# Kernel optimization log

Measured on AMD Instinct MI355X. Metric: run time of the kernel, lower is better.

## Reference

```python
import jax, jax.numpy as jnp
import numpy as np

B, S, D, H = 2, 2048, 1024, 16
DK = D // H


def setup_inputs() -> dict:
    key = jax.random.key(0)
    ks = jax.random.split(key, 12)
    scale = 1.0 / np.sqrt(D)
    inp = {
        "query": jax.random.normal(ks[0], (B, S, D), jnp.float32),
        "key": jax.random.normal(ks[1], (B, S, D), jnp.float32),
        "value": jax.random.normal(ks[2], (B, S, D), jnp.float32),
        "mask": jax.random.randint(ks[3], (B, 1, S, S), 0, 2, jnp.int32),
        "Wq": jax.random.normal(ks[4], (D, D), jnp.float32) * scale,
        "bq": jnp.zeros((D,), jnp.float32),
        "Wk": jax.random.normal(ks[5], (D, D), jnp.float32) * scale,
        "bk": jnp.zeros((D,), jnp.float32),
        "Wv": jax.random.normal(ks[6], (D, D), jnp.float32) * scale,
        "bv": jnp.zeros((D,), jnp.float32),
        "Wo": jax.random.normal(ks[7], (D, D), jnp.float32) * scale,
        "bo": jnp.zeros((D,), jnp.float32),
    }
    return inp


def reference(query, key, value, mask, Wq, bq, Wk, bk, Wv, bv, Wo, bo):
    # Linear projections (dropout is identity in eval mode)
    q = query @ Wq + bq          # (B,S,D)
    k = key @ Wk + bk
    v = value @ Wv + bv

    # split heads: (B,S,D) -> (B,H,S,DK)
    def split(x):
        return x.reshape(B, S, H, DK).transpose(0, 2, 1, 3)

    q, k, v = split(q), split(k), split(v)

    scores = jnp.einsum("bhqd,bhkd->bhqk", q, k) / jnp.sqrt(jnp.float32(DK))
    scores = jnp.where(mask == 0, jnp.float32(-1e9), scores)
    p_attn = jax.nn.softmax(scores, axis=-1)   # (B,H,S,S)

    att = jnp.einsum("bhqk,bhkd->bhqd", p_attn, v)  # (B,H,S,DK)
    merged = att.transpose(0, 2, 1, 3).reshape(B, S, D)
    return merged @ Wo + bo
```

## Files before the change

kernel.cpp:

```cpp
#include <hip/hip_runtime.h>
#include <hip/hip_bf16.h>
#include <cstdint>
#include <cstddef>


#define B_ 2
#define S_ 2048
#define D_ 1024
#define H_ 16
#define M_ 4096

typedef unsigned short u16;
typedef __attribute__((ext_vector_type(8))) short bf16x8;
typedef __attribute__((ext_vector_type(8))) unsigned short u16x8;
typedef __attribute__((ext_vector_type(4))) unsigned short u16x4;
typedef __attribute__((ext_vector_type(4))) unsigned int u32x4;
typedef __attribute__((ext_vector_type(4))) float f32x4;
typedef __attribute__((ext_vector_type(4))) int i32x4;

#define QSCALE 0.18033688011112042f

__device__ __forceinline__ u16 f2bf(float f) {
  __hip_bfloat16 h = __float2bfloat16(f);
  return *reinterpret_cast<u16*>(&h);
}

__device__ __forceinline__ unsigned cvtpk(float lo, float hi) {
  unsigned r;
  asm("v_cvt_pk_bf16_f32 %0, %1, %2" : "=v"(r) : "v"(lo), "v"(hi));
  return r;
}

__device__ __forceinline__ void gload_lds16(const void* g, void* l) {
  __builtin_amdgcn_global_load_lds((const __attribute__((address_space(1))) void*)g,
                                   (__attribute__((address_space(3))) void*)l, 16, 0, 0);
}

__global__ __launch_bounds__(256) void k_convert(const float* __restrict__ q, const float* __restrict__ k,
                                                 const float* __restrict__ v,
                                                 u16* __restrict__ xq, u16* __restrict__ xk, u16* __restrict__ xv) {
  int z = blockIdx.y;
  const float* src = (z == 0) ? q : (z == 1) ? k : v;
  u16* dst = (z == 0) ? xq : (z == 1) ? xk : xv;
  size_t i = ((size_t)blockIdx.x * 256 + threadIdx.x) * 8;
  f32x4 a = *(const f32x4*)(src + i);
  f32x4 b = *(const f32x4*)(src + i + 4);
  u16x8 o;
  o[0]=f2bf(a[0]); o[1]=f2bf(a[1]); o[2]=f2bf(a[2]); o[3]=f2bf(a[3]);
  o[4]=f2bf(b[0]); o[5]=f2bf(b[1]); o[6]=f2bf(b[2]); o[7]=f2bf(b[3]);
  *(u16x8*)(dst + i) = o;
}

__global__ __launch_bounds__(256) void k_transposeW(const float* __restrict__ w0, const float* __restrict__ w1,
                                                    const float* __restrict__ w2, const float* __restrict__ w3,
                                                    u16* __restrict__ t0, u16* __restrict__ t1,
                                                    u16* __restrict__ t2, u16* __restrict__ t3) {
  int z = blockIdx.z;
  const float* W = (z==0)?w0:(z==1)?w1:(z==2)?w2:w3;
  u16* Wt = (z==0)?t0:(z==1)?t1:(z==2)?t2:t3;
  __shared__ float tile[32][33];
  int tx = threadIdx.x & 31, ty = threadIdx.x >> 5;
  int bx = blockIdx.x * 32, by = blockIdx.y * 32;
  #pragma unroll
  for (int p = 0; p < 4; ++p)
    tile[ty + p*8][tx] = W[(size_t)(by + ty + p*8) * D_ + bx + tx];
  __syncthreads();
  #pragma unroll
  for (int p = 0; p < 4; ++p)
    Wt[(size_t)(bx + ty + p*8) * D_ + by + tx] = f2bf(tile[tx][ty + p*8]);
}

__global__ __launch_bounds__(256) void k_packmask(const int* __restrict__ mask, u16* __restrict__ out) {
  size_t t = (size_t)blockIdx.x * 256 + threadIdx.x;
  const int* p = mask + t * 64;
  unsigned wds0 = 0, wds1 = 0, wds2 = 0, wds3 = 0;
  #pragma unroll
  for (int c = 0; c < 16; ++c) {
    i32x4 v = *(const i32x4*)(p + c*4);
    #pragma unroll
    for (int e = 0; e < 4; ++e) {
      const int k = c*4 + e;
      const int lcw = (k >> 3) & 3;
      const int ni = ((k >> 4) & 2) | ((k >> 2) & 1);
      const unsigned bit = 1u << (4*ni + (k & 3));
      if (v[e]) {
        if (lcw == 0) wds0 |= bit; else if (lcw == 1) wds1 |= bit;
        else if (lcw == 2) wds2 |= bit; else wds3 |= bit;
      }
    }
  }
  u16x4 w; w[0] = (u16)wds0; w[1] = (u16)wds1; w[2] = (u16)wds2; w[3] = (u16)wds3;
  *(u16x4*)(out + t*4) = w;
}

template<int CMODE>
__device__ __forceinline__ void gemm_core(const u16* __restrict__ A, const u16* __restrict__ Bt,
                                          const float* __restrict__ bias, void* __restrict__ Cv, float scale) {
  __shared__ u16 As[128*64];
  __shared__ u16 Bs[128*64];
  const int t = threadIdx.x;
  const int l = t & 63, w = t >> 6;
  const int wr = w >> 1, wc = w & 1;
  const int lr = l & 15, lc = l >> 4;
  const int bm = blockIdx.x, bn = blockIdx.y;
  f32x4 acc[4][4];
  #pragma unroll
  for (int i = 0; i < 4; ++i)
    #pragma unroll
    for (int j = 0; j < 4; ++j) { f32x4 z = {0.f,0.f,0.f,0.f}; acc[i][j] = z; }
  const int srow = t >> 3;
  const u16* ga = A  + (size_t)(bm*128 + srow) * 1024;
  const u16* gb = Bt + (size_t)(bn*128 + srow) * 1024;
  u16* la = &As[t*8];
  u16* lb = &Bs[t*8];
  for (int kt = 0; kt < 16; ++kt) {
    const int ko = kt * 64;
    __syncthreads();
    #pragma unroll
    for (int i = 0; i < 4; ++i) {
      int blk = (t & 7) ^ ((i*32 + srow) & 7);
      gload_lds16(ga + (size_t)(i*32)*1024 + ko + blk*8, la + i*2048);
      gload_lds16(gb + (size_t)(i*32)*1024 + ko + blk*8, lb + i*2048);
    }
    __syncthreads();
    #pragma unroll
    for (int ks = 0; ks < 2; ++ks) {
      bf16x8 af[4], bfr[4];
      #pragma unroll
      for (int mi = 0; mi < 4; ++mi)
        af[mi]  = *(const bf16x8*)&As[(wr*64 + mi*16 + lr)*64 + (((ks*4 + lc) ^ (lr & 7))*8)];
      #pragma unroll
      for (int ni = 0; ni < 4; ++ni)
        bfr[ni] = *(const bf16x8*)&Bs[(wc*64 + ni*16 + lr)*64 + (((ks*4 + lc) ^ (lr & 7))*8)];
      #pragma unroll
      for (int mi = 0; mi < 4; ++mi)
        #pragma unroll
        for (int ni = 0; ni < 4; ++ni)
          acc[mi][ni] = __builtin_amdgcn_mfma_f32_16x16x32_bf16(af[mi], bfr[ni], acc[mi][ni], 0, 0, 0);
    }
  }
  #pragma unroll
  for (int ni = 0; ni < 4; ++ni) {
    int gcol = bn*128 + wc*64 + ni*16 + lr;
    float bv = bias[gcol];
    #pragma unroll
    for (int mi = 0; mi < 4; ++mi) {
      int grow = bm*128 + wr*64 + mi*16 + lc*4;
      if (CMODE == 2) {
        u16x4 pk;
        #pragma unroll
        for (int j = 0; j < 4; ++j) pk[j] = f2bf((acc[mi][ni][j] + bv) * scale);
        *(u16x4*)&((u16*)Cv)[(size_t)gcol * M_ + grow] = pk;
      } else {
        #pragma unroll
        for (int j = 0; j < 4; ++j) {
          float v = (acc[mi][ni][j] + bv) * scale;
          if (CMODE == 0) ((u16*)Cv)[(size_t)(grow + j) * 1024 + gcol] = f2bf(v);
          else            ((float*)Cv)[(size_t)(grow + j) * 1024 + gcol] = v;
        }
      }
    }
  }
}

__global__ __launch_bounds__(256) void k_gemm_qkv(const u16* Xq, const u16* Xk, const u16* Xv,
                                                  const u16* Wqt, const u16* Wkt, const u16* Wvt,
                                                  const float* bq, const float* bk, const float* bv,
                                                  u16* Qo, u16* Ko, u16* Vt, float qscale) {
  int z = blockIdx.z;
  if (z == 0)      gemm_core<0>(Xq, Wqt, bq, Qo, qscale);
  else if (z == 1) gemm_core<0>(Xk, Wkt, bk, Ko, 1.f);
  else             gemm_core<2>(Xv, Wvt, bv, Vt, 1.f);
}

__global__ __launch_bounds__(256) void k_gemm_out(const u16* Aatt, const u16* Wot, const float* bo, float* out) {
  gemm_core<1>(Aatt, Wot, bo, out, 1.f);
}

__global__ __launch_bounds__(256) void k_attn(const u16* __restrict__ Q, const u16* __restrict__ Kb,
                                              const u16* __restrict__ Vt,
                                              const u16* __restrict__ mbw,
                                              u16* __restrict__ attb) {
  __shared__ u16 Ks[3*4096];
  __shared__ u16 Vs[2*4096];
  const int t = threadIdx.x, l = t & 63, w = t >> 6;
  const int lr = l & 15, lc = l >> 4;
  const int qt = blockIdx.x, h = blockIdx.y, b = blockIdx.z;
  const int r0 = t >> 3;
  const int c0 = (t & 7) ^ (r0 & 7);
  const int pr0 = ((r0 & 12) << 1) | ((r0 & 16) >> 2) | (r0 & 3);
  const u16* kp0 = Kb + (size_t)(b*S_ + pr0)*D_ + h*64 + c0*8;
  const u16* vp0 = Vt + (size_t)(h*64 + r0)*M_ + b*S_ + c0*8;

  gload_lds16(Q + (size_t)(b*S_ + qt*64 + r0)*D_      + h*64 + c0*8, &Ks[t*8]);
  gload_lds16(Q + (size_t)(b*S_ + qt*64 + r0 + 32)*D_ + h*64 + c0*8, &Ks[2048 + t*8]);
  __syncthreads();
  const int qrow = w*16 + lr;
  const int sw0 = ((lc     ) ^ (lr & 7)) * 8;
  const int sw1 = ((4 + lc ) ^ (lr & 7)) * 8;
  bf16x8 aq0 = *(const bf16x8*)&Ks[qrow*64 + sw0];
  bf16x8 aq1 = *(const bf16x8*)&Ks[qrow*64 + sw1];
  __syncthreads();
  gload_lds16(kp0,                                 &Ks[t*8]);
  gload_lds16(kp0 + (size_t)32*D_,                 &Ks[2048 + t*8]);
  gload_lds16(vp0,                                 &Vs[t*8]);
  gload_lds16(vp0 + (size_t)32*M_,                 &Vs[2048 + t*8]);
  gload_lds16(kp0 + (size_t)64*D_,                 &Ks[4096 + t*8]);
  gload_lds16(kp0 + (size_t)64*D_ + (size_t)32*D_, &Ks[4096 + 2048 + t*8]);

  f32x4 lsv = {0.f,0.f,0.f,0.f};
  f32x4 o[4];
  #pragma unroll
  for (int ni = 0; ni < 4; ++ni) { f32x4 z = {0.f,0.f,0.f,0.f}; o[ni] = z; }
  const u16* mptr = mbw + (size_t)(b*S_ + qt*64 + qrow)*128 + lc;
  int kc = 0, kn = 4096, knn = 8192;

  #pragma unroll 2
  for (int kt = 0; kt < 32; ++kt) {
    if (kt == 31) asm volatile("s_waitcnt vmcnt(0)");
    else          asm volatile("s_waitcnt vmcnt(2)");
    __builtin_amdgcn_s_barrier();
    __builtin_amdgcn_sched_barrier(0);
    unsigned mw = mptr[kt*4];
    if (kt < 31) {
      const size_t ko = (size_t)(kt + 1) * 64;
      const int vb = ((kt + 1) & 1) * 4096;
      gload_lds16(vp0 + ko,                    &Vs[vb + t*8]);
      gload_lds16(vp0 + ko + (size_t)32*M_,    &Vs[vb + 2048 + t*8]);
    }
    if (kt < 30) {
      const size_t ko2 = (size_t)(kt + 2) * 64;
      gload_lds16(kp0 + ko2*D_,                 &Ks[knn + t*8]);
      gload_lds16(kp0 + ko2*D_ + (size_t)32*D_, &Ks[knn + 2048 + t*8]);
    }
    f32x4 s[4];
    #pragma unroll
    for (int ni = 0; ni < 4; ++ni) { f32x4 z = {0.f,0.f,0.f,0.f}; s[ni] = z; }
    __builtin_amdgcn_s_setprio(1);
    #pragma unroll
    for (int ni = 0; ni < 4; ++ni) {
      bf16x8 bk0 = *(const bf16x8*)&Ks[kc + (ni*16 + lr)*64 + sw0];
      bf16x8 bk1 = *(const bf16x8*)&Ks[kc + (ni*16 + lr)*64 + sw1];
      s[ni] = __builtin_amdgcn_mfma_f32_16x16x32_bf16(bk0, aq0, s[ni], 0, 0, 0);
      s[ni] = __builtin_amdgcn_mfma_f32_16x16x32_bf16(bk1, aq1, s[ni], 0, 0, 0);
    }
    __builtin_amdgcn_s_setprio(0);
    #pragma unroll
    for (int ni = 0; ni < 4; ++ni)
      #pragma unroll
      for (int j = 0; j < 4; ++j) {
        float pv = __builtin_amdgcn_exp2f(s[ni][j]);
        int bm = ((int)(mw << (31 - (4*ni + j)))) >> 31;
        union { float f; int i; } u; u.f = pv; u.i &= bm;
        s[ni][j] = u.f;
      }
    lsv += (s[0] + s[1]) + (s[2] + s[3]);
    u32x4 pw0, pw1;
    pw0[0] = cvtpk(s[0][0], s[0][1]); pw0[1] = cvtpk(s[0][2], s[0][3]);
    pw0[2] = cvtpk(s[1][0], s[1][1]); pw0[3] = cvtpk(s[1][2], s[1][3]);
    pw1[0] = cvtpk(s[2][0], s[2][1]); pw1[1] = cvtpk(s[2][2], s[2][3]);
    pw1[2] = cvtpk(s[3][0], s[3][1]); pw1[3] = cvtpk(s[3][2], s[3][3]);
    bf16x8 pa0 = __builtin_bit_cast(bf16x8, pw0);
    bf16x8 pa1 = __builtin_bit_cast(bf16x8, pw1);
    const int vc = (kt & 1) * 4096;
    __builtin_amdgcn_s_setprio(1);
    #pragma unroll
    for (int ni = 0; ni < 4; ++ni) {
      bf16x8 bv0 = *(const bf16x8*)&Vs[vc + (ni*16 + lr)*64 + sw0];
      o[ni] = __builtin_amdgcn_mfma_f32_16x16x32_bf16(pa0, bv0, o[ni], 0, 0, 0);
    }
    #pragma unroll
    for (int ni = 0; ni < 4; ++ni) {
      bf16x8 bv1 = *(const bf16x8*)&Vs[vc + (ni*16 + lr)*64 + sw1];
      o[ni] = __builtin_amdgcn_mfma_f32_16x16x32_bf16(pa1, bv1, o[ni], 0, 0, 0);
    }
    __builtin_amdgcn_s_setprio(0);
    int tmp = kc; kc = kn; kn = knn; knn = tmp;
  }
  float tot = (lsv[0] + lsv[1]) + (lsv[2] + lsv[3]);
  tot += __shfl_xor(tot, 16);
  tot += __shfl_xor(tot, 32);
  float rl[4];
  #pragma unroll
  for (int j = 0; j < 4; ++j)
    rl[j] = 1.f / __shfl(tot, lc*4 + j);
  #pragma unroll
  for (int ni = 0; ni < 4; ++ni)
    #pragma unroll
    for (int j = 0; j < 4; ++j) {
      int orow = qt*64 + w*16 + lc*4 + j, dcol = ni*16 + lr;
      attb[(size_t)(b*S_ + orow)*D_ + h*64 + dcol] = f2bf(o[ni][j] * rl[j]);
    }
}

extern "C" void kernel_launch(void* const* d_in, const int* in_sizes, int n_in,
                              void* d_out, int out_size, void* d_ws, size_t ws_size,
                              hipStream_t stream) {
  (void)in_sizes; (void)n_in; (void)out_size; (void)ws_size;
  const float* query = (const float*)d_in[0];
  const float* key   = (const float*)d_in[1];
  const float* value = (const float*)d_in[2];
  const int*   mask  = (const int*)d_in[3];
  const float* Wq = (const float*)d_in[4];
  const float* bq = (const float*)d_in[5];
  const float* Wk = (const float*)d_in[6];
  const float* bk = (const float*)d_in[7];
  const float* Wv = (const float*)d_in[8];
  const float* bv = (const float*)d_in[9];
  const float* Wo = (const float*)d_in[10];
  const float* bo = (const float*)d_in[11];
  float* out = (float*)d_out;
  char* ws = (char*)d_ws;
  const size_t MB = 1024 * 1024;
  u16* Xq  = (u16*)(ws + 0*MB);
  u16* Xk  = (u16*)(ws + 8*MB);
  u16* Xv  = (u16*)(ws + 16*MB);
  u16* Wqt = (u16*)(ws + 24*MB);
  u16* Wkt = (u16*)(ws + 26*MB);
  u16* Wvt = (u16*)(ws + 28*MB);
  u16* Wot = (u16*)(ws + 30*MB);
  u16* Qb  = (u16*)(ws + 32*MB);
  u16* Kb  = (u16*)(ws + 40*MB);
  u16* Vtb = (u16*)(ws + 48*MB);
  u16* mbits = (u16*)(ws + 56*MB);
  u16* attb = (u16*)(ws + 0*MB);

  k_convert  <<<dim3(2048, 3),     256, 0, stream>>>(query, key, value, Xq, Xk, Xv);
  k_transposeW<<<dim3(32, 32, 4),  256, 0, stream>>>(Wq, Wk, Wv, Wo, Wqt, Wkt, Wvt, Wot);
  k_packmask <<<dim3(512),         256, 0, stream>>>(mask, mbits);
  k_gemm_qkv <<<dim3(32, 8, 3),    256, 0, stream>>>(Xq, Xk, Xv, Wqt, Wkt, Wvt, bq, bk, bv,
                                                     Qb, Kb, Vtb, QSCALE);
  k_attn     <<<dim3(32, 16, 2),   256, 0, stream>>>(Qb, Kb, Vtb, mbits, attb);
  k_gemm_out <<<dim3(32, 8),       256, 0, stream>>>(attb, Wot, bo, out);
}
```

Baseline: 153.3 us.

## Double-buffer GEMM LDS tiles, shrink N tile, compute softmax row sums via MFMA

The GEMM core now double-buffers its A/B LDS tiles, issuing the next k-tile's global-to-LDS loads before computing the current one. It also shrinks the output tile from 128x128 to 128x64, doubling the grid to raise occupancy and wave count. Separately, the attention kernel computes softmax row sums with an extra MFMA against a ones vector instead of per-lane vector adds plus shuffles. This adds LDS use and two MFMAs per iteration, and reduces per-block data reuse in the GEMM.

```diff
diff --git a/kernel.cpp b/kernel.cpp
--- a/kernel.cpp
+++ b/kernel.cpp
@@ -93,59 +93,71 @@
   *(u16x4*)(out + t*4) = w;
 }
 
-template<int CMODE>
+template<int CMODE, int MI, int NI>
 __device__ __forceinline__ void gemm_core(const u16* __restrict__ A, const u16* __restrict__ Bt,
                                           const float* __restrict__ bias, void* __restrict__ Cv, float scale) {
-  __shared__ u16 As[128*64];
-  __shared__ u16 Bs[128*64];
+  constexpr int ASZ = MI*32*64;
+  constexpr int BSZ = NI*32*64;
+  __shared__ u16 As[2*ASZ];
+  __shared__ u16 Bs[2*BSZ];
   const int t = threadIdx.x;
   const int l = t & 63, w = t >> 6;
   const int wr = w >> 1, wc = w & 1;
   const int lr = l & 15, lc = l >> 4;
   const int bm = blockIdx.x, bn = blockIdx.y;
-  f32x4 acc[4][4];
-  #pragma unroll
-  for (int i = 0; i < 4; ++i)
-    #pragma unroll
-    for (int j = 0; j < 4; ++j) { f32x4 z = {0.f,0.f,0.f,0.f}; acc[i][j] = z; }
+  f32x4 acc[MI][NI];
+  #pragma unroll
+  for (int i = 0; i < MI; ++i)
+    #pragma unroll
+    for (int j = 0; j < NI; ++j) { f32x4 z = {0.f,0.f,0.f,0.f}; acc[i][j] = z; }
   const int srow = t >> 3;
-  const u16* ga = A  + (size_t)(bm*128 + srow) * 1024;
-  const u16* gb = Bt + (size_t)(bn*128 + srow) * 1024;
-  u16* la = &As[t*8];
-  u16* lb = &Bs[t*8];
+  const int blkx = (t & 7) ^ (srow & 7);
+  const u16* ga = A  + (size_t)(bm*(MI*32) + srow)*1024 + blkx*8;
+  const u16* gb = Bt + (size_t)(bn*(NI*32) + srow)*1024 + blkx*8;
+
+#define GSTAGE(KT, BUF) do {                                                        \
+    _Pragma("unroll")                                                               \
+    for (int i = 0; i < MI; ++i)                                                    \
+      gload_lds16(ga + (size_t)(i*32)*1024 + (KT)*64, &As[(BUF)*ASZ + i*2048 + t*8]); \
+    _Pragma("unroll")                                                               \
+    for (int i = 0; i < NI; ++i)                                                    \
+      gload_lds16(gb + (size_t)(i*32)*1024 + (KT)*64, &Bs[(BUF)*BSZ + i*2048 + t*8]); \
+  } while (0)
+
+  GSTAGE(0, 0);
+  int cur = 0;
   for (int kt = 0; kt < 16; ++kt) {
-    const int ko = kt * 64;
-    __syncthreads();
-    #pragma unroll
-    for (int i = 0; i < 4; ++i) {
-      int blk = (t & 7) ^ ((i*32 + srow) & 7);
-      gload_lds16(ga + (size_t)(i*32)*1024 + ko + blk*8, la + i*2048);
-      gload_lds16(gb + (size_t)(i*32)*1024 + ko + blk*8, lb + i*2048);
-    }
-    __syncthreads();
+    asm volatile("s_waitcnt vmcnt(0)");
+    __builtin_amdgcn_s_barrier();
+    __builtin_amdgcn_sched_barrier(0);
+    if (kt < 15) GSTAGE(kt + 1, cur ^ 1);
+    __builtin_amdgcn_s_setprio(1);
     #pragma unroll
     for (int ks = 0; ks < 2; ++ks) {
-      bf16x8 af[4], bfr[4];
+      bf16x8 af[MI], bfr[NI];
       #pragma unroll
-      for (int mi = 0; mi < 4; ++mi)
-        af[mi]  = *(const bf16x8*)&As[(wr*64 + mi*16 + lr)*64 + (((ks*4 + lc) ^ (lr & 7))*8)];
+      for (int mi = 0; mi < MI; ++mi)
+        af[mi]  = *(const bf16x8*)&As[cur*ASZ + (wr*(MI*16) + mi*16 + lr)*64 + (((ks*4 + lc) ^ (lr & 7))*8)];
       #pragma unroll
-      for (int ni = 0; ni < 4; ++ni)
-        bfr[ni] = *(const bf16x8*)&Bs[(wc*64 + ni*16 + lr)*64 + (((ks*4 + lc) ^ (lr & 7))*8)];
+      for (int ni = 0; ni < NI; ++ni)
+        bfr[ni] = *(const bf16x8*)&Bs[cur*BSZ + (wc*(NI*16) + ni*16 + lr)*64 + (((ks*4 + lc) ^ (lr & 7))*8)];
       #pragma unroll
-      for (int mi = 0; mi < 4; ++mi)
+      for (int mi = 0; mi < MI; ++mi)
         #pragma unroll
-        for (int ni = 0; ni < 4; ++ni)
+        for (int ni = 0; ni < NI; ++ni)
           acc[mi][ni] = __builtin_amdgcn_mfma_f32_16x16x32_bf16(af[mi], bfr[ni], acc[mi][ni], 0, 0, 0);
     }
+    __builtin_amdgcn_s_setprio(0);
+    cur ^= 1;
   }
-  #pragma unroll
-  for (int ni = 0; ni < 4; ++ni) {
-    int gcol = bn*128 + wc*64 + ni*16 + lr;
+#undef GSTAGE
+  #pragma unroll
+  for (int ni = 0; ni < NI; ++ni) {
+    int gcol = bn*(NI*32) + wc*(NI*16) + ni*16 + lr;
     float bv = bias[gcol];
     #pragma unroll
-    for (int mi = 0; mi < 4; ++mi) {
-      int grow = bm*128 + wr*64 + mi*16 + lc*4;
+    for (int mi = 0; mi < MI; ++mi) {
+      int grow = bm*(MI*32) + wr*(MI*16) + mi*16 + lc*4;
       if (CMODE == 2) {
         u16x4 pk;
         #pragma unroll
@@ -168,13 +180,13 @@
                                                   const float* bq, const float* bk, const float* bv,
                                                   u16* Qo, u16* Ko, u16* Vt, float qscale) {
   int z = blockIdx.z;
-  if (z == 0)      gemm_core<0>(Xq, Wqt, bq, Qo, qscale);
-  else if (z == 1) gemm_core<0>(Xk, Wkt, bk, Ko, 1.f);
-  else             gemm_core<2>(Xv, Wvt, bv, Vt, 1.f);
+  if (z == 0)      gemm_core<0,4,2>(Xq, Wqt, bq, Qo, qscale);
+  else if (z == 1) gemm_core<0,4,2>(Xk, Wkt, bk, Ko, 1.f);
+  else             gemm_core<2,4,2>(Xv, Wvt, bv, Vt, 1.f);
 }
 
 __global__ __launch_bounds__(256) void k_gemm_out(const u16* Aatt, const u16* Wot, const float* bo, float* out) {
-  gemm_core<1>(Aatt, Wot, bo, out, 1.f);
+  gemm_core<1,4,2>(Aatt, Wot, bo, out, 1.f);
 }
 
 __global__ __launch_bounds__(256) void k_attn(const u16* __restrict__ Q, const u16* __restrict__ Kb,
@@ -208,7 +220,9 @@
   gload_lds16(kp0 + (size_t)64*D_,                 &Ks[4096 + t*8]);
   gload_lds16(kp0 + (size_t)64*D_ + (size_t)32*D_, &Ks[4096 + 2048 + t*8]);
 
-  f32x4 lsv = {0.f,0.f,0.f,0.f};
+  const short one_bf = (short)0x3F80;
+  const bf16x8 onesf = {one_bf,one_bf,one_bf,one_bf,one_bf,one_bf,one_bf,one_bf};
+  f32x4 ls = {0.f,0.f,0.f,0.f};
   f32x4 o[4];
   #pragma unroll
   for (int ni = 0; ni < 4; ++ni) { f32x4 z = {0.f,0.f,0.f,0.f}; o[ni] = z; }
@@ -254,7 +268,6 @@
         union { float f; int i; } u; u.f = pv; u.i &= bm;
         s[ni][j] = u.f;
       }
-    lsv += (s[0] + s[1]) + (s[2] + s[3]);
     u32x4 pw0, pw1;
     pw0[0] = cvtpk(s[0][0], s[0][1]); pw0[1] = cvtpk(s[0][2], s[0][3]);
     pw0[2] = cvtpk(s[1][0], s[1][1]); pw0[3] = cvtpk(s[1][2], s[1][3]);
@@ -264,6 +277,8 @@
     bf16x8 pa1 = __builtin_bit_cast(bf16x8, pw1);
     const int vc = (kt & 1) * 4096;
     __builtin_amdgcn_s_setprio(1);
+    ls = __builtin_amdgcn_mfma_f32_16x16x32_bf16(pa0, onesf, ls, 0, 0, 0);
+    ls = __builtin_amdgcn_mfma_f32_16x16x32_bf16(pa1, onesf, ls, 0, 0, 0);
     #pragma unroll
     for (int ni = 0; ni < 4; ++ni) {
       bf16x8 bv0 = *(const bf16x8*)&Vs[vc + (ni*16 + lr)*64 + sw0];
@@ -277,13 +292,9 @@
     __builtin_amdgcn_s_setprio(0);
     int tmp = kc; kc = kn; kn = knn; knn = tmp;
   }
-  float tot = (lsv[0] + lsv[1]) + (lsv[2] + lsv[3]);
-  tot += __shfl_xor(tot, 16);
-  tot += __shfl_xor(tot, 32);
   float rl[4];
   #pragma unroll
-  for (int j = 0; j < 4; ++j)
-    rl[j] = 1.f / __shfl(tot, lc*4 + j);
+  for (int j = 0; j < 4; ++j) rl[j] = 1.f / ls[j];
   #pragma unroll
   for (int ni = 0; ni < 4; ++ni)
     #pragma unroll
@@ -328,8 +339,8 @@
   k_convert  <<<dim3(2048, 3),     256, 0, stream>>>(query, key, value, Xq, Xk, Xv);
   k_transposeW<<<dim3(32, 32, 4),  256, 0, stream>>>(Wq, Wk, Wv, Wo, Wqt, Wkt, Wvt, Wot);
   k_packmask <<<dim3(512),         256, 0, stream>>>(mask, mbits);
-  k_gemm_qkv <<<dim3(32, 8, 3),    256, 0, stream>>>(Xq, Xk, Xv, Wqt, Wkt, Wvt, bq, bk, bv,
+  k_gemm_qkv <<<dim3(32, 16, 3),   256, 0, stream>>>(Xq, Xk, Xv, Wqt, Wkt, Wvt, bq, bk, bv,
                                                      Qb, Kb, Vtb, QSCALE);
   k_attn     <<<dim3(32, 16, 2),   256, 0, stream>>>(Qb, Kb, Vtb, mbits, attb);
-  k_gemm_out <<<dim3(32, 8),       256, 0, stream>>>(attb, Wot, bo, out);
-}
+  k_gemm_out <<<dim3(32, 16),      256, 0, stream>>>(attb, Wot, bo, out);
+}
```

Result: slower. 179.6 us (+17.1%).
